# Optimization experiments

Hardware: AMD Instinct MI355X
Metric: run time of the kernel (lower is better)

Reference implementation:

```python
import jax, jax.numpy as jnp
import numpy as np

NEG_SLOPE = 0.01  # torch leaky_relu default

def _lrelu(x):
    return jax.nn.leaky_relu(x, NEG_SLOPE)

def _l2norm(x, axis):
    # torch F.normalize(p=2, eps=1e-12)
    n = jnp.linalg.norm(x, axis=axis, keepdims=True)
    return x / jnp.maximum(n, 1e-12)

def setup_inputs() -> dict:
    key = jax.random.key(0)
    ks = jax.random.split(key, 12)
    Nda, Nq, C, Din, Dout = 10000, 64, 1024, 128, 256
    target_adj = (jax.random.uniform(ks[0], (Nda, Nda)) < 0.002).astype(jnp.float32)
    query_adj = (jax.random.uniform(ks[1], (Nq, Nq)) < 0.2).astype(jnp.float32)
    node_features_da = jax.random.normal(ks[2], (Nda, Din), dtype=jnp.float32)
    node_features_q = jax.random.normal(ks[3], (Nq, Din), dtype=jnp.float32)
    candidate_set = jax.random.randint(ks[4], (C,), 0, Nda)
    candidate_adj = (jax.random.uniform(ks[5], (C, C)) < 0.01).astype(jnp.float32)
    s_in = 1.0 / np.sqrt(Din).astype(np.float32)
    s_out = 1.0 / np.sqrt(Dout).astype(np.float32)
    W1_da = jax.random.normal(ks[6], (Din, Dout), dtype=jnp.float32) * s_in
    W1_q = jax.random.normal(ks[7], (Din, Dout), dtype=jnp.float32) * s_in
    W2_da = jax.random.normal(ks[8], (Dout, Dout), dtype=jnp.float32) * s_out
    W2_q = jax.random.normal(ks[9], (Dout, Dout), dtype=jnp.float32) * s_out
    threshold = jnp.float32(0.2)
    return {"target_adj": target_adj, "node_features_da": node_features_da,
            "query_adj": query_adj, "node_features_q": node_features_q,
            "candidate_set": candidate_set, "candidate_adj": candidate_adj,
            "threshold": threshold, "W1_da": W1_da, "W1_q": W1_q,
            "W2_da": W2_da, "W2_q": W2_q}

def _cross_cosine(q, da, candidate_set):
    # cosine similarity between each query node and each candidate target node: [Nq, C]
    return _l2norm(q, 1) @ _l2norm(da[candidate_set], 1).T

def reference(target_adj, node_features_da, query_adj, node_features_q,
              candidate_set, candidate_adj, threshold, W1_da, W1_q, W2_da, W2_q):
    # layer 1: GCN propagation on both graphs (gcn(adj,x) = adj @ x @ W)
    da1 = _lrelu(target_adj @ (node_features_da @ W1_da))   # [Nda, D]
    q1 = _lrelu(query_adj @ (node_features_q @ W1_q))       # [Nq, D]
    c1 = _cross_cosine(q1, da1, candidate_set)               # [Nq, C]
    pre_da1 = da1[candidate_set]                             # [C, D]
    # NOTE: da1[candidate_set].data = ... mutates a temporary in torch -> no-op on da1
    att_da1 = _lrelu(da1)                                    # dropout in eval = identity
    h1_q = c1 @ pre_da1                                      # [Nq, D]
    att_q1 = _lrelu(q1 + _l2norm(h1_q, 0))
    # layer 2
    da2 = _lrelu(target_adj @ (att_da1 @ W2_da))
    q2 = _lrelu(query_adj @ (att_q1 @ W2_q))
    c2 = _cross_cosine(q2, da2, candidate_set)
    pre_da2 = da2[candidate_set]
    att_da2 = _lrelu(da2)                                    # in-place update is again a no-op
    h2_q = c2 @ pre_da2
    att_q2 = _lrelu(q2 + _l2norm(h2_q, 0))
    # graph-level matching score per target node
    emb = jnp.mean(att_q2, axis=0, keepdims=True)            # [1, D]
    num = att_da2 @ emb[0]                                   # [Nda]
    den = jnp.maximum(jnp.linalg.norm(att_da2, axis=1) * jnp.linalg.norm(emb), 1e-8)
    end = (num / den)[None, :]                               # [1, Nda]
    # threshold selection expressed with a mask (jit-safe, same math: excluded
    # rows/cols are zero and do not affect L2 norms, sums, or the trace)
    m = (end[0] > threshold).astype(att_da2.dtype)           # [Nda]
    F_ = att_da2 * m[:, None]
    re_adj = F_ @ F_.T                                       # [Nda, Nda]
    nor_re = _l2norm(re_adj, 1) * target_adj                 # elementwise with original adj
    cnt = jnp.sum(m)
    total = jnp.sum(nor_re)
    tr = jnp.trace(nor_re)
    has = cnt > 0
    pre_avg_degree = jnp.where(has, total / jnp.maximum(cnt, 1.0), 0.0)
    pre_avg_nodes = jnp.where(has, tr, 0.0)
    pre_density = jnp.where(has, 2.0 * total / (tr * (tr - 1.0) + 1e-4), 0.0)
    return (end, att_da2, att_q2, pre_avg_degree, pre_density, pre_avg_nodes)
```

## Files before the change

kernel.cpp:

```cpp
#include <hip/hip_runtime.h>

constexpr int NDA = 10000;
constexpr int NQ  = 64;
constexpr int CND = 1024;
constexpr int DIN = 128;
constexpr int D   = 256;
constexpr int CAP = 96;
constexpr int NB_BIG = ((NDA + 63) / 64) * (D / 64);

#define LRELU(x) ((x) >= 0.f ? (x) : 0.01f * (x))

__device__ __forceinline__ float wave_red64(float v) {
#pragma unroll
    for (int o = 32; o; o >>= 1) v += __shfl_down(v, o);
    return v;
}

struct GemmSmem { float As[32][68]; float Bs[32][68]; };

template <bool RELU_A, bool RELU_C>
__device__ __forceinline__ void gemm_body(GemmSmem& sm, int bx, int by,
                                          const float* __restrict__ A,
                                          const float* __restrict__ B,
                                          float* __restrict__ C,
                                          int M, int N, int K) {
    const int bm = bx * 64, bn = by * 64;
    const int tid = threadIdx.x;
    const int tx = tid & 15, ty = tid >> 4;
    const int lm = tid >> 2, lk = (tid & 3) * 8;
    const int kb = tid >> 3, nb = (tid & 7) * 8;
    const bool aValid = (bm + lm) < M;
    const float* aPtr = A + (size_t)(bm + lm) * K + lk;
    const float* bPtr = B + (size_t)kb * N + bn + nb;
    float4 ra0 = make_float4(0.f, 0.f, 0.f, 0.f), ra1 = ra0, rb0, rb1;
    if (aValid) { ra0 = *(const float4*)aPtr; ra1 = *(const float4*)(aPtr + 4); }
    rb0 = *(const float4*)bPtr;
    rb1 = *(const float4*)(bPtr + 4);
    float acc[4][4] = {};
    for (int k0 = 0; k0 < K; k0 += 32) {
        float4 wa0 = ra0, wa1 = ra1, wb0 = rb0, wb1 = rb1;
        if (RELU_A) {
            wa0.x = LRELU(wa0.x); wa0.y = LRELU(wa0.y); wa0.z = LRELU(wa0.z); wa0.w = LRELU(wa0.w);
            wa1.x = LRELU(wa1.x); wa1.y = LRELU(wa1.y); wa1.z = LRELU(wa1.z); wa1.w = LRELU(wa1.w);
        }
        sm.As[lk + 0][lm] = wa0.x; sm.As[lk + 1][lm] = wa0.y;
        sm.As[lk + 2][lm] = wa0.z; sm.As[lk + 3][lm] = wa0.w;
        sm.As[lk + 4][lm] = wa1.x; sm.As[lk + 5][lm] = wa1.y;
        sm.As[lk + 6][lm] = wa1.z; sm.As[lk + 7][lm] = wa1.w;
        *(float4*)&sm.Bs[kb][nb]     = wb0;
        *(float4*)&sm.Bs[kb][nb + 4] = wb1;
        __syncthreads();
        if (k0 + 32 < K) {
            if (aValid) {
                ra0 = *(const float4*)(aPtr + k0 + 32);
                ra1 = *(const float4*)(aPtr + k0 + 36);
            }
            rb0 = *(const float4*)(bPtr + (size_t)(k0 + 32) * N);
            rb1 = *(const float4*)(bPtr + (size_t)(k0 + 32) * N + 4);
        }
#pragma unroll
        for (int kk = 0; kk < 32; kk++) {
            float av[4], bv[4];
#pragma unroll
            for (int i = 0; i < 4; i++) av[i] = sm.As[kk][ty * 4 + i];
#pragma unroll
            for (int j = 0; j < 4; j++) bv[j] = sm.Bs[kk][tx * 4 + j];
#pragma unroll
            for (int i = 0; i < 4; i++)
#pragma unroll
                for (int j = 0; j < 4; j++) acc[i][j] += av[i] * bv[j];
        }
        __syncthreads();
    }
#pragma unroll
    for (int i = 0; i < 4; i++) {
        int r = bm + ty * 4 + i;
        if (r < M) {
            float4 v = make_float4(acc[i][0], acc[i][1], acc[i][2], acc[i][3]);
            if (RELU_C) { v.x = LRELU(v.x); v.y = LRELU(v.y); v.z = LRELU(v.z); v.w = LRELU(v.w); }
            *(float4*)(C + (size_t)r * N + bn + tx * 4) = v;
        }
    }
}

__device__ __forceinline__ void csr_body(const float* __restrict__ adj,
                                         int* __restrict__ cols,
                                         int* __restrict__ rowcnt, int row) {
    __shared__ int scnt;
    if (threadIdx.x == 0) scnt = 0;
    __syncthreads();
    const float4* rp = (const float4*)(adj + (size_t)row * NDA);
    for (int i = threadIdx.x; i < NDA / 4; i += 256) {
        float4 v = rp[i];
        if (v.x != 0.f) { int s = atomicAdd(&scnt, 1); if (s < CAP) cols[row * CAP + s] = 4 * i; }
        if (v.y != 0.f) { int s = atomicAdd(&scnt, 1); if (s < CAP) cols[row * CAP + s] = 4 * i + 1; }
        if (v.z != 0.f) { int s = atomicAdd(&scnt, 1); if (s < CAP) cols[row * CAP + s] = 4 * i + 2; }
        if (v.w != 0.f) { int s = atomicAdd(&scnt, 1); if (s < CAP) cols[row * CAP + s] = 4 * i + 3; }
    }
    __syncthreads();
    if (threadIdx.x == 0) rowcnt[row] = min(scnt, CAP);
}

__device__ __forceinline__ void spmm_body(const int* __restrict__ cols,
                                          const int* __restrict__ rowcnt,
                                          const float* __restrict__ X,
                                          float* __restrict__ out1,
                                          float* __restrict__ out2, int row) {
    int d = threadIdx.x;
    int cnt = rowcnt[row];
    __shared__ int sc[CAP];
    if (d < cnt) sc[d] = cols[row * CAP + d];
    __syncthreads();
    float a0 = 0.f, a1 = 0.f, a2 = 0.f, a3 = 0.f;
    int k = 0;
    for (; k + 4 <= cnt; k += 4) {
        a0 += X[(size_t)sc[k + 0] * D + d];
        a1 += X[(size_t)sc[k + 1] * D + d];
        a2 += X[(size_t)sc[k + 2] * D + d];
        a3 += X[(size_t)sc[k + 3] * D + d];
    }
    for (; k < cnt; k++) a0 += X[(size_t)sc[k] * D + d];
    float v = LRELU(a0 + a1 + a2 + a3);
    out1[(size_t)row * D + d] = v;
    if (out2) out2[(size_t)row * D + d] = LRELU(v);
}

__global__ __launch_bounds__(256) void stage0_kernel(const float* __restrict__ adj,
                                                     int* __restrict__ cols,
                                                     int* __restrict__ rowcnt,
                                                     const float* __restrict__ Fda,
                                                     const float* __restrict__ W1da,
                                                     float* __restrict__ X1,
                                                     const float* __restrict__ Fq,
                                                     const float* __restrict__ W1q,
                                                     float* __restrict__ Xq) {
    __shared__ GemmSmem gs;
    int bid = blockIdx.x;
    if (bid < NB_BIG) {
        gemm_body<false, false>(gs, bid >> 2, bid & 3, Fda, W1da, X1, NDA, D, DIN);
    } else if (bid < NB_BIG + 4) {
        gemm_body<false, false>(gs, 0, bid - NB_BIG, Fq, W1q, Xq, NQ, D, DIN);
    } else {
        csr_body(adj, cols, rowcnt, bid - (NB_BIG + 4));
    }
}

__global__ __launch_bounds__(256) void stage_sg_kernel(const int* __restrict__ cols,
                                                       const int* __restrict__ rowcnt,
                                                       const float* __restrict__ X,
                                                       float* __restrict__ out1,
                                                       float* __restrict__ out2,
                                                       const float* __restrict__ Aq,
                                                       const float* __restrict__ Bq,
                                                       float* __restrict__ Cq) {
    __shared__ GemmSmem gs;
    int bid = blockIdx.x;
    if (bid < 4) {
        gemm_body<false, true>(gs, 0, bid, Aq, Bq, Cq, NQ, D, NQ);
    } else {
        spmm_body(cols, rowcnt, X, out1, out2, bid - 4);
    }
}

__global__ __launch_bounds__(256) void stage4_kernel(const float* __restrict__ da1,
                                                     const float* __restrict__ W2da,
                                                     float* __restrict__ Y2,
                                                     const float* __restrict__ aq1,
                                                     const float* __restrict__ W2q,
                                                     float* __restrict__ Zq) {
    __shared__ GemmSmem gs;
    int bid = blockIdx.x;
    if (bid < NB_BIG) {
        gemm_body<true, false>(gs, bid >> 2, bid & 3, da1, W2da, Y2, NDA, D, D);
    } else {
        gemm_body<false, false>(gs, 0, bid - NB_BIG, aq1, W2q, Zq, NQ, D, D);
    }
}

__global__ __launch_bounds__(256) void gemmH_kernel(const float* __restrict__ A,
                                                    const float* __restrict__ B,
                                                    float* __restrict__ C) {
    __shared__ GemmSmem gs;
    gemm_body<false, false>(gs, blockIdx.x, blockIdx.y, A, B, C, NDA, D, D);
}

__global__ __launch_bounds__(256) void cross_kernel(const float* __restrict__ q,
                                                    const float* __restrict__ da,
                                                    const int* __restrict__ cand,
                                                    float* __restrict__ hpart) {
    __shared__ float qs[D];
    __shared__ float cmw[256];
    __shared__ int sci[256];
    __shared__ float red[4];
    __shared__ float sqn;
    int r = blockIdx.x, qr = blockIdx.y;
    int d = threadIdx.x;
    float qv = q[r * D + d];
    qs[d] = qv;
    sci[d] = cand[qr * 256 + d];
    float p = wave_red64(qv * qv);
    int w = d >> 6, lane = d & 63;
    if (lane == 0) red[w] = p;
    __syncthreads();
    if (d == 0) sqn = fmaxf(sqrtf(red[0] + red[1] + red[2] + red[3]), 1e-12f);
    __syncthreads();
    float qn = sqn;
    {
        const float4* ap = (const float4*)(da + (size_t)sci[d] * D);
        float dot = 0.f, sq = 0.f;
#pragma unroll 8
        for (int k = 0; k < D / 4; k++) {
            float4 v = ap[k];
            dot += qs[4 * k] * v.x + qs[4 * k + 1] * v.y + qs[4 * k + 2] * v.z + qs[4 * k + 3] * v.w;
            sq  += v.x * v.x + v.y * v.y + v.z * v.z + v.w * v.w;
        }
        cmw[d] = dot / (qn * fmaxf(sqrtf(sq), 1e-12f));
    }
    __syncthreads();
    float a0 = 0.f, a1 = 0.f, a2 = 0.f, a3 = 0.f, a4 = 0.f, a5 = 0.f, a6 = 0.f, a7 = 0.f;
    for (int c = 0; c < 256; c += 8) {
        a0 += cmw[c + 0] * da[(size_t)sci[c + 0] * D + d];
        a1 += cmw[c + 1] * da[(size_t)sci[c + 1] * D + d];
        a2 += cmw[c + 2] * da[(size_t)sci[c + 2] * D + d];
        a3 += cmw[c + 3] * da[(size_t)sci[c + 3] * D + d];
        a4 += cmw[c + 4] * da[(size_t)sci[c + 4] * D + d];
        a5 += cmw[c + 5] * da[(size_t)sci[c + 5] * D + d];
        a6 += cmw[c + 6] * da[(size_t)sci[c + 6] * D + d];
        a7 += cmw[c + 7] * da[(size_t)sci[c + 7] * D + d];
    }
    hpart[((size_t)qr * NQ + r) * D + d] = ((a0 + a1) + (a2 + a3)) + ((a4 + a5) + (a6 + a7));
}

__global__ __launch_bounds__(256) void attq_kernel(const float* __restrict__ q,
                                                   const float* __restrict__ hpart,
                                                   float* __restrict__ attq,
                                                   float* __restrict__ emb) {
    int d = threadIdx.x;
    float hv[NQ];
    float ss = 0.f;
#pragma unroll
    for (int r = 0; r < NQ; r++) {
        float h = hpart[(size_t)r * D + d]
                + hpart[(size_t)(NQ + r) * D + d]
                + hpart[(size_t)(2 * NQ + r) * D + d]
                + hpart[(size_t)(3 * NQ + r) * D + d];
        hv[r] = h;
        ss += h * h;
    }
    float inv = 1.f / fmaxf(sqrtf(ss), 1e-12f);
    float es = 0.f;
#pragma unroll
    for (int r = 0; r < NQ; r++) {
        float v = q[r * D + d] + hv[r] * inv;
        v = LRELU(v);
        attq[r * D + d] = v;
        es += v;
    }
    if (emb) {
        float e = es * (1.f / (float)NQ);
        emb[d] = e;
        float p = wave_red64(e * e);
        __shared__ float red[4];
        int w = d >> 6, lane = d & 63;
        if (lane == 0) red[w] = p;
        __syncthreads();
        if (d == 0) emb[D] = sqrtf(red[0] + red[1] + red[2] + red[3]);
    }
}

__global__ __launch_bounds__(256) void end_kernel(const float* __restrict__ A,
                                                  const float* __restrict__ emb,
                                                  const float* __restrict__ thr_p,
                                                  float* __restrict__ endv,
                                                  float* __restrict__ m,
                                                  float* __restrict__ cnt) {
    __shared__ float se[D];
    __shared__ float scnt;
    int d = threadIdx.x;
    se[d] = emb[d];
    if (d == 0) scnt = 0.f;
    __syncthreads();
    float embn = emb[D];
    float thr = *thr_p;
    int w = d >> 6, lane = d & 63;
    int row = blockIdx.x * 4 + w;
    const float* ar = A + (size_t)row * D;
    float num = 0.f, sq = 0.f;
#pragma unroll
    for (int s = 0; s < 4; s++) {
        float v = ar[lane + 64 * s];
        num += v * se[lane + 64 * s];
        sq += v * v;
    }
#pragma unroll
    for (int o = 32; o; o >>= 1) { num += __shfl_down(num, o); sq += __shfl_down(sq, o); }
    if (lane == 0) {
        float den = fmaxf(sqrtf(sq) * embn, 1e-8f);
        float e = num / den;
        endv[row] = e;
        float mv = e > thr ? 1.f : 0.f;
        m[row] = mv;
        if (mv != 0.f) atomicAdd(&scnt, 1.f);
    }
    __syncthreads();
    if (d == 0 && scnt != 0.f) atomicAdd(cnt, scnt);
}

constexpr int GCHUNK = 400;
__global__ __launch_bounds__(256) void G_kernel(const float* __restrict__ A,
                                                const float* __restrict__ m,
                                                float* __restrict__ G) {
    __shared__ float SA[8][64], SB[8][64];
    int ti = blockIdx.x >> 2, tj = blockIdx.x & 3;
    int base = blockIdx.y * GCHUNK;
    int tid = threadIdx.x;
    int tx = tid & 15, ty = tid >> 4;
    float acc[4][4] = {};
    for (int g0 = 0; g0 < GCHUNK; g0 += 8) {
        for (int l = tid; l < 512; l += 256) {
            int rr = l >> 6, c = l & 63;
            int r = base + g0 + rr;
            float mv = m[r];
            SA[rr][c] = A[(size_t)r * D + ti * 64 + c] * mv;
            SB[rr][c] = A[(size_t)r * D + tj * 64 + c];
        }
        __syncthreads();
#pragma unroll
        for (int rr = 0; rr < 8; rr++) {
            float av[4], bv[4];
#pragma unroll
            for (int i = 0; i < 4; i++) av[i] = SA[rr][ty * 4 + i];
#pragma unroll
            for (int j = 0; j < 4; j++) bv[j] = SB[rr][tx * 4 + j];
#pragma unroll
            for (int i = 0; i < 4; i++)
#pragma unroll
                for (int j = 0; j < 4; j++) acc[i][j] += av[i] * bv[j];
        }
        __syncthreads();
    }
#pragma unroll
    for (int i = 0; i < 4; i++)
#pragma unroll
        for (int j = 0; j < 4; j++)
            atomicAdd(&G[(ti * 64 + ty * 4 + i) * D + tj * 64 + tx * 4 + j], acc[i][j]);
}

__global__ __launch_bounds__(256) void final_kernel(const int* __restrict__ cols,
                                                    const int* __restrict__ rowcnt,
                                                    const float* __restrict__ m,
                                                    const float* __restrict__ A,
                                                    const float* __restrict__ H,
                                                    double* __restrict__ total,
                                                    double* __restrict__ tr) {
    int i = blockIdx.x;
    if (m[i] == 0.f) return;
    int d = threadIdx.x;
    int cnt = rowcnt[i];
    __shared__ int sc[CAP];
    __shared__ float smask[CAP];
    __shared__ int sdiag;
    __shared__ float r1[4], r2[4], r3[4];
    if (d == 0) sdiag = 0;
    if (d < cnt) {
        int j = cols[i * CAP + d];
        sc[d] = j;
        smask[d] = m[j];
        if (j == i) sdiag = 1;
    }
    __syncthreads();
    float av = A[(size_t)i * D + d];
    float hv = H[(size_t)i * D + d];
    float sd = 0.f;
    for (int k = 0; k < cnt; k++)
        if (smask[k] != 0.f) sd += A[(size_t)sc[k] * D + d];
    float p1 = av * sd, p2 = av * hv, p3 = av * av;
#pragma unroll
    for (int o = 32; o; o >>= 1) {
        p1 += __shfl_down(p1, o);
        p2 += __shfl_down(p2, o);
        p3 += __shfl_down(p3, o);
    }
    int w = d >> 6, lane = d & 63;
    if (lane == 0) { r1[w] = p1; r2[w] = p2; r3[w] = p3; }
    __syncthreads();
    if (d == 0) {
        float num  = r1[0] + r1[1] + r1[2] + r1[3];
        float den2 = r2[0] + r2[1] + r2[2] + r2[3];
        float self = r3[0] + r3[1] + r3[2] + r3[3];
        float denom = fmaxf(sqrtf(den2), 1e-12f);
        double inv = 1.0 / (double)denom;
        if (num != 0.f) atomicAdd(total, (double)num * inv);
        if (sdiag) atomicAdd(tr, (double)self * inv);
    }
}

__global__ void scalars_kernel(const float* __restrict__ cnt,
                               const double* __restrict__ total,
                               const double* __restrict__ tr,
                               float* __restrict__ out) {
    float c = *cnt;
    float T = (float)*total;
    float R = (float)*tr;
    bool has = c > 0.f;
    out[0] = has ? (T / fmaxf(c, 1.f)) : 0.f;
    out[1] = has ? (2.f * T / (R * (R - 1.f) + 1e-4f)) : 0.f;
    out[2] = has ? R : 0.f;
}

extern "C" void kernel_launch(void* const* d_in, const int* in_sizes, int n_in,
                              void* d_out, int out_size, void* d_ws, size_t ws_size,
                              hipStream_t stream) {
    (void)in_sizes; (void)n_in; (void)out_size; (void)ws_size;
    const float* adj  = (const float*)d_in[0];
    const float* Fda  = (const float*)d_in[1];
    const float* Qadj = (const float*)d_in[2];
    const float* Fq   = (const float*)d_in[3];
    const int*   cand = (const int*)d_in[4];
    const float* thr  = (const float*)d_in[6];
    const float* W1da = (const float*)d_in[7];
    const float* W1q  = (const float*)d_in[8];
    const float* W2da = (const float*)d_in[9];
    const float* W2q  = (const float*)d_in[10];

    float* out = (float*)d_out;
    float* o_end    = out;
    float* o_attda2 = out + NDA;
    float* o_attq2  = out + NDA + (size_t)NDA * D;
    float* o_sc     = o_attq2 + NQ * D;

    char* w = (char*)d_ws;
    size_t off = 0;
    auto alloc = [&](size_t b) { size_t r = off; off += (b + 255) & ~(size_t)255; return r; };
    float* bufA = (float*)(w + alloc((size_t)NDA * D * 4));
    float* bufB = (float*)(w + alloc((size_t)NDA * D * 4));
    float* bufC = (float*)(w + alloc((size_t)NDA * D * 4));
    int* colsb   = (int*)(w + alloc((size_t)NDA * CAP * 4));
    int* rowcntb = (int*)(w + alloc((size_t)NDA * 4));
    float* mbuf  = (float*)(w + alloc((size_t)NDA * 4));
    char* zbase = w + alloc(262144 + 256);
    float* Gb    = (float*)zbase;
    float* cntb  = (float*)(zbase + 262144);
    double* totb = (double*)(zbase + 262144 + 8);
    double* trb  = (double*)(zbase + 262144 + 16);
    float* xq   = (float*)(w + alloc((size_t)NQ * D * 4));
    float* q1b  = (float*)(w + alloc((size_t)NQ * D * 4));
    float* aq1  = (float*)(w + alloc((size_t)NQ * D * 4));
    float* q2b  = (float*)(w + alloc((size_t)NQ * D * 4));
    float* hpart = (float*)(w + alloc((size_t)4 * NQ * D * 4));
    float* embb = (float*)(w + alloc((size_t)(D + 1) * 4));

    hipMemsetAsync(zbase, 0, 262144 + 256, stream);

    stage0_kernel<<<NB_BIG + 4 + NDA, 256, 0, stream>>>(adj, colsb, rowcntb,
                                                        Fda, W1da, bufA,
                                                        Fq, W1q, xq);
    stage_sg_kernel<<<NDA + 4, 256, 0, stream>>>(colsb, rowcntb, bufA, bufB, (float*)nullptr,
                                                 Qadj, xq, q1b);
    cross_kernel<<<dim3(NQ, 4), 256, 0, stream>>>(q1b, bufB, cand, hpart);
    attq_kernel<<<1, 256, 0, stream>>>(q1b, hpart, aq1, (float*)nullptr);
    stage4_kernel<<<NB_BIG + 4, 256, 0, stream>>>(bufB, W2da, bufA, aq1, W2q, xq);
    stage_sg_kernel<<<NDA + 4, 256, 0, stream>>>(colsb, rowcntb, bufA, bufC, o_attda2,
                                                 Qadj, xq, q2b);
    cross_kernel<<<dim3(NQ, 4), 256, 0, stream>>>(q2b, bufC, cand, hpart);
    attq_kernel<<<1, 256, 0, stream>>>(q2b, hpart, o_attq2, embb);
    end_kernel<<<NDA / 4, 256, 0, stream>>>(o_attda2, embb, thr, o_end, mbuf, cntb);
    G_kernel<<<dim3(16, NDA / GCHUNK), 256, 0, stream>>>(o_attda2, mbuf, Gb);
    gemmH_kernel<<<dim3((NDA + 63) / 64, D / 64), 256, 0, stream>>>(o_attda2, Gb, bufB);
    final_kernel<<<NDA, 256, 0, stream>>>(colsb, rowcntb, mbuf, o_attda2, bufB, totb, trb);
    scalars_kernel<<<1, 1, 0, stream>>>(cntb, totb, trb, o_sc);
}
```

Before: 1.050 ms.

## Fuse pipeline into one cooperative persistent kernel with grid syncs

Replaces the chain of separate kernel launches with a single cooperative persistent megakernel that walks through the stages with grid-wide syncs, sharing one shared-memory union. Multi-launch code is kept as a fallback. It also splits the G accumulation into per-chunk partials plus a reduction instead of global atomics, and merges the first cross-similarity with the second-layer GEMM. The aim is to cut launch gaps and atomic contention, at the cost of grid sync overhead and lower occupancy for the large stages.

```diff
diff --git a/kernel.cpp b/kernel.cpp
--- a/kernel.cpp
+++ b/kernel.cpp
@@ -1,4 +1,7 @@
 #include <hip/hip_runtime.h>
+#include <hip/hip_cooperative_groups.h>
+
+namespace cg = cooperative_groups;
 
 constexpr int NDA = 10000;
 constexpr int NQ  = 64;
@@ -7,6 +10,8 @@
 constexpr int D   = 256;
 constexpr int CAP = 96;
 constexpr int NB_BIG = ((NDA + 63) / 64) * (D / 64);
+constexpr int NCHUNK = 16;
+constexpr int GCHUNK = 640;
 
 #define LRELU(x) ((x) >= 0.f ? (x) : 0.01f * (x))
 
@@ -16,7 +21,18 @@
     return v;
 }
 
-struct GemmSmem { float As[32][68]; float Bs[32][68]; };
+struct GemmSmem  { float As[32][68]; float Bs[32][68]; };
+struct CrossSmem { float qs[D]; float cmw[256]; int sci[256]; float red[4]; float sqn; };
+struct SpmmSmem  { int sc[CAP]; };
+struct CsrSmem   { int scnt; };
+struct EndSmem   { float se[D]; float scnt; };
+struct FinalSmem { int sc[CAP]; float smask[CAP]; int sdiag; float r1[4], r2[4], r3[4]; };
+struct GpSmem    { float SA[8][64]; float SB[8][64]; };
+struct AttqSmem  { float red[4]; };
+union SMem {
+    GemmSmem g; CrossSmem c; SpmmSmem s; CsrSmem z;
+    EndSmem e; FinalSmem f; GpSmem gp; AttqSmem a;
+};
 
 template <bool RELU_A, bool RELU_C>
 __device__ __forceinline__ void gemm_body(GemmSmem& sm, int bx, int by,
@@ -83,175 +99,111 @@
     }
 }
 
-__device__ __forceinline__ void csr_body(const float* __restrict__ adj,
+__device__ __forceinline__ void csr_body(CsrSmem& sm, const float* __restrict__ adj,
                                          int* __restrict__ cols,
                                          int* __restrict__ rowcnt, int row) {
-    __shared__ int scnt;
-    if (threadIdx.x == 0) scnt = 0;
+    if (threadIdx.x == 0) sm.scnt = 0;
     __syncthreads();
     const float4* rp = (const float4*)(adj + (size_t)row * NDA);
     for (int i = threadIdx.x; i < NDA / 4; i += 256) {
         float4 v = rp[i];
-        if (v.x != 0.f) { int s = atomicAdd(&scnt, 1); if (s < CAP) cols[row * CAP + s] = 4 * i; }
-        if (v.y != 0.f) { int s = atomicAdd(&scnt, 1); if (s < CAP) cols[row * CAP + s] = 4 * i + 1; }
-        if (v.z != 0.f) { int s = atomicAdd(&scnt, 1); if (s < CAP) cols[row * CAP + s] = 4 * i + 2; }
-        if (v.w != 0.f) { int s = atomicAdd(&scnt, 1); if (s < CAP) cols[row * CAP + s] = 4 * i + 3; }
-    }
-    __syncthreads();
-    if (threadIdx.x == 0) rowcnt[row] = min(scnt, CAP);
-}
-
-__device__ __forceinline__ void spmm_body(const int* __restrict__ cols,
+        if (v.x != 0.f) { int s = atomicAdd(&sm.scnt, 1); if (s < CAP) cols[row * CAP + s] = 4 * i; }
+        if (v.y != 0.f) { int s = atomicAdd(&sm.scnt, 1); if (s < CAP) cols[row * CAP + s] = 4 * i + 1; }
+        if (v.z != 0.f) { int s = atomicAdd(&sm.scnt, 1); if (s < CAP) cols[row * CAP + s] = 4 * i + 2; }
+        if (v.w != 0.f) { int s = atomicAdd(&sm.scnt, 1); if (s < CAP) cols[row * CAP + s] = 4 * i + 3; }
+    }
+    __syncthreads();
+    if (threadIdx.x == 0) rowcnt[row] = min(sm.scnt, CAP);
+}
+
+__device__ __forceinline__ void spmm_body(SpmmSmem& sm, const int* __restrict__ cols,
                                           const int* __restrict__ rowcnt,
                                           const float* __restrict__ X,
                                           float* __restrict__ out1,
                                           float* __restrict__ out2, int row) {
     int d = threadIdx.x;
     int cnt = rowcnt[row];
-    __shared__ int sc[CAP];
-    if (d < cnt) sc[d] = cols[row * CAP + d];
+    if (d < cnt) sm.sc[d] = cols[row * CAP + d];
     __syncthreads();
     float a0 = 0.f, a1 = 0.f, a2 = 0.f, a3 = 0.f;
     int k = 0;
     for (; k + 4 <= cnt; k += 4) {
-        a0 += X[(size_t)sc[k + 0] * D + d];
-        a1 += X[(size_t)sc[k + 1] * D + d];
-        a2 += X[(size_t)sc[k + 2] * D + d];
-        a3 += X[(size_t)sc[k + 3] * D + d];
-    }
-    for (; k < cnt; k++) a0 += X[(size_t)sc[k] * D + d];
+        a0 += X[(size_t)sm.sc[k + 0] * D + d];
+        a1 += X[(size_t)sm.sc[k + 1] * D + d];
+        a2 += X[(size_t)sm.sc[k + 2] * D + d];
+        a3 += X[(size_t)sm.sc[k + 3] * D + d];
+    }
+    for (; k < cnt; k++) a0 += X[(size_t)sm.sc[k] * D + d];
     float v = LRELU(a0 + a1 + a2 + a3);
     out1[(size_t)row * D + d] = v;
     if (out2) out2[(size_t)row * D + d] = LRELU(v);
 }
 
-__global__ __launch_bounds__(256) void stage0_kernel(const float* __restrict__ adj,
-                                                     int* __restrict__ cols,
-                                                     int* __restrict__ rowcnt,
-                                                     const float* __restrict__ Fda,
-                                                     const float* __restrict__ W1da,
-                                                     float* __restrict__ X1,
-                                                     const float* __restrict__ Fq,
-                                                     const float* __restrict__ W1q,
-                                                     float* __restrict__ Xq) {
-    __shared__ GemmSmem gs;
-    int bid = blockIdx.x;
-    if (bid < NB_BIG) {
-        gemm_body<false, false>(gs, bid >> 2, bid & 3, Fda, W1da, X1, NDA, D, DIN);
-    } else if (bid < NB_BIG + 4) {
-        gemm_body<false, false>(gs, 0, bid - NB_BIG, Fq, W1q, Xq, NQ, D, DIN);
-    } else {
-        csr_body(adj, cols, rowcnt, bid - (NB_BIG + 4));
-    }
-}
-
-__global__ __launch_bounds__(256) void stage_sg_kernel(const int* __restrict__ cols,
-                                                       const int* __restrict__ rowcnt,
-                                                       const float* __restrict__ X,
-                                                       float* __restrict__ out1,
-                                                       float* __restrict__ out2,
-                                                       const float* __restrict__ Aq,
-                                                       const float* __restrict__ Bq,
-                                                       float* __restrict__ Cq) {
-    __shared__ GemmSmem gs;
-    int bid = blockIdx.x;
-    if (bid < 4) {
-        gemm_body<false, true>(gs, 0, bid, Aq, Bq, Cq, NQ, D, NQ);
-    } else {
-        spmm_body(cols, rowcnt, X, out1, out2, bid - 4);
-    }
-}
-
-__global__ __launch_bounds__(256) void stage4_kernel(const float* __restrict__ da1,
-                                                     const float* __restrict__ W2da,
-                                                     float* __restrict__ Y2,
-                                                     const float* __restrict__ aq1,
-                                                     const float* __restrict__ W2q,
-                                                     float* __restrict__ Zq) {
-    __shared__ GemmSmem gs;
-    int bid = blockIdx.x;
-    if (bid < NB_BIG) {
-        gemm_body<true, false>(gs, bid >> 2, bid & 3, da1, W2da, Y2, NDA, D, D);
-    } else {
-        gemm_body<false, false>(gs, 0, bid - NB_BIG, aq1, W2q, Zq, NQ, D, D);
-    }
-}
-
-__global__ __launch_bounds__(256) void gemmH_kernel(const float* __restrict__ A,
-                                                    const float* __restrict__ B,
-                                                    float* __restrict__ C) {
-    __shared__ GemmSmem gs;
-    gemm_body<false, false>(gs, blockIdx.x, blockIdx.y, A, B, C, NDA, D, D);
-}
-
-__global__ __launch_bounds__(256) void cross_kernel(const float* __restrict__ q,
-                                                    const float* __restrict__ da,
-                                                    const int* __restrict__ cand,
-                                                    float* __restrict__ hpart) {
-    __shared__ float qs[D];
-    __shared__ float cmw[256];
-    __shared__ int sci[256];
-    __shared__ float red[4];
-    __shared__ float sqn;
-    int r = blockIdx.x, qr = blockIdx.y;
+__device__ __forceinline__ void cross_body(CrossSmem& sm, const float* __restrict__ q,
+                                           const float* __restrict__ da,
+                                           const int* __restrict__ cand,
+                                           float* __restrict__ hpart,
+                                           int r, int qr) {
     int d = threadIdx.x;
     float qv = q[r * D + d];
-    qs[d] = qv;
-    sci[d] = cand[qr * 256 + d];
+    sm.qs[d] = qv;
+    sm.sci[d] = cand[qr * 256 + d];
     float p = wave_red64(qv * qv);
     int w = d >> 6, lane = d & 63;
-    if (lane == 0) red[w] = p;
-    __syncthreads();
-    if (d == 0) sqn = fmaxf(sqrtf(red[0] + red[1] + red[2] + red[3]), 1e-12f);
-    __syncthreads();
-    float qn = sqn;
+    if (lane == 0) sm.red[w] = p;
+    __syncthreads();
+    if (d == 0) sm.sqn = fmaxf(sqrtf(sm.red[0] + sm.red[1] + sm.red[2] + sm.red[3]), 1e-12f);
+    __syncthreads();
+    float qn = sm.sqn;
     {
-        const float4* ap = (const float4*)(da + (size_t)sci[d] * D);
+        const float4* ap = (const float4*)(da + (size_t)sm.sci[d] * D);
         float dot = 0.f, sq = 0.f;
 #pragma unroll 8
         for (int k = 0; k < D / 4; k++) {
             float4 v = ap[k];
-            dot += qs[4 * k] * v.x + qs[4 * k + 1] * v.y + qs[4 * k + 2] * v.z + qs[4 * k + 3] * v.w;
+            dot += sm.qs[4 * k] * v.x + sm.qs[4 * k + 1] * v.y + sm.qs[4 * k + 2] * v.z + sm.qs[4 * k + 3] * v.w;
             sq  += v.x * v.x + v.y * v.y + v.z * v.z + v.w * v.w;
         }
-        cmw[d] = dot / (qn * fmaxf(sqrtf(sq), 1e-12f));
+        sm.cmw[d] = dot / (qn * fmaxf(sqrtf(sq), 1e-12f));
     }
     __syncthreads();
     float a0 = 0.f, a1 = 0.f, a2 = 0.f, a3 = 0.f, a4 = 0.f, a5 = 0.f, a6 = 0.f, a7 = 0.f;
     for (int c = 0; c < 256; c += 8) {
-        a0 += cmw[c + 0] * da[(size_t)sci[c + 0] * D + d];
-        a1 += cmw[c + 1] * da[(size_t)sci[c + 1] * D + d];
-        a2 += cmw[c + 2] * da[(size_t)sci[c + 2] * D + d];
-        a3 += cmw[c + 3] * da[(size_t)sci[c + 3] * D + d];
-        a4 += cmw[c + 4] * da[(size_t)sci[c + 4] * D + d];
-        a5 += cmw[c + 5] * da[(size_t)sci[c + 5] * D + d];
-        a6 += cmw[c + 6] * da[(size_t)sci[c + 6] * D + d];
-        a7 += cmw[c + 7] * da[(size_t)sci[c + 7] * D + d];
+        a0 += sm.cmw[c + 0] * da[(size_t)sm.sci[c + 0] * D + d];
+        a1 += sm.cmw[c + 1] * da[(size_t)sm.sci[c + 1] * D + d];
+        a2 += sm.cmw[c + 2] * da[(size_t)sm.sci[c + 2] * D + d];
+        a3 += sm.cmw[c + 3] * da[(size_t)sm.sci[c + 3] * D + d];
+        a4 += sm.cmw[c + 4] * da[(size_t)sm.sci[c + 4] * D + d];
+        a5 += sm.cmw[c + 5] * da[(size_t)sm.sci[c + 5] * D + d];
+        a6 += sm.cmw[c + 6] * da[(size_t)sm.sci[c + 6] * D + d];
+        a7 += sm.cmw[c + 7] * da[(size_t)sm.sci[c + 7] * D + d];
     }
     hpart[((size_t)qr * NQ + r) * D + d] = ((a0 + a1) + (a2 + a3)) + ((a4 + a5) + (a6 + a7));
 }
 
-__global__ __launch_bounds__(256) void attq_kernel(const float* __restrict__ q,
-                                                   const float* __restrict__ hpart,
-                                                   float* __restrict__ attq,
-                                                   float* __restrict__ emb) {
+__device__ __forceinline__ void attq_body(AttqSmem& sm, const float* __restrict__ q,
+                                          const float* __restrict__ hpart,
+                                          float* __restrict__ attq,
+                                          float* __restrict__ emb) {
     int d = threadIdx.x;
-    float hv[NQ];
     float ss = 0.f;
-#pragma unroll
+#pragma unroll 4
     for (int r = 0; r < NQ; r++) {
         float h = hpart[(size_t)r * D + d]
                 + hpart[(size_t)(NQ + r) * D + d]
                 + hpart[(size_t)(2 * NQ + r) * D + d]
                 + hpart[(size_t)(3 * NQ + r) * D + d];
-        hv[r] = h;
         ss += h * h;
     }
     float inv = 1.f / fmaxf(sqrtf(ss), 1e-12f);
     float es = 0.f;
-#pragma unroll
+#pragma unroll 4
     for (int r = 0; r < NQ; r++) {
-        float v = q[r * D + d] + hv[r] * inv;
+        float h = hpart[(size_t)r * D + d]
+                + hpart[(size_t)(NQ + r) * D + d]
+                + hpart[(size_t)(2 * NQ + r) * D + d]
+                + hpart[(size_t)(3 * NQ + r) * D + d];
+        float v = q[r * D + d] + h * inv;
         v = LRELU(v);
         attq[r * D + d] = v;
         es += v;
@@ -260,36 +212,33 @@
         float e = es * (1.f / (float)NQ);
         emb[d] = e;
         float p = wave_red64(e * e);
-        __shared__ float red[4];
         int w = d >> 6, lane = d & 63;
-        if (lane == 0) red[w] = p;
-        __syncthreads();
-        if (d == 0) emb[D] = sqrtf(red[0] + red[1] + red[2] + red[3]);
-    }
-}
-
-__global__ __launch_bounds__(256) void end_kernel(const float* __restrict__ A,
-                                                  const float* __restrict__ emb,
-                                                  const float* __restrict__ thr_p,
-                                                  float* __restrict__ endv,
-                                                  float* __restrict__ m,
-                                                  float* __restrict__ cnt) {
-    __shared__ float se[D];
-    __shared__ float scnt;
+        if (lane == 0) sm.red[w] = p;
+        __syncthreads();
+        if (d == 0) emb[D] = sqrtf(sm.red[0] + sm.red[1] + sm.red[2] + sm.red[3]);
+    }
+}
+
+__device__ __forceinline__ void end_body(EndSmem& sm, const float* __restrict__ A,
+                                         const float* __restrict__ emb,
+                                         const float* __restrict__ thr_p,
+                                         float* __restrict__ endv,
+                                         float* __restrict__ m,
+                                         float* __restrict__ cnt, int quad) {
     int d = threadIdx.x;
-    se[d] = emb[d];
-    if (d == 0) scnt = 0.f;
+    sm.se[d] = emb[d];
+    if (d == 0) sm.scnt = 0.f;
     __syncthreads();
     float embn = emb[D];
     float thr = *thr_p;
     int w = d >> 6, lane = d & 63;
-    int row = blockIdx.x * 4 + w;
+    int row = quad * 4 + w;
     const float* ar = A + (size_t)row * D;
     float num = 0.f, sq = 0.f;
 #pragma unroll
     for (int s = 0; s < 4; s++) {
         float v = ar[lane + 64 * s];
-        num += v * se[lane + 64 * s];
+        num += v * sm.se[lane + 64 * s];
         sq += v * v;
     }
 #pragma unroll
@@ -300,19 +249,17 @@
         endv[row] = e;
         float mv = e > thr ? 1.f : 0.f;
         m[row] = mv;
-        if (mv != 0.f) atomicAdd(&scnt, 1.f);
-    }
-    __syncthreads();
-    if (d == 0 && scnt != 0.f) atomicAdd(cnt, scnt);
-}
-
-constexpr int GCHUNK = 400;
-__global__ __launch_bounds__(256) void G_kernel(const float* __restrict__ A,
-                                                const float* __restrict__ m,
-                                                float* __restrict__ G) {
-    __shared__ float SA[8][64], SB[8][64];
-    int ti = blockIdx.x >> 2, tj = blockIdx.x & 3;
-    int base = blockIdx.y * GCHUNK;
+        if (mv != 0.f) atomicAdd(&sm.scnt, 1.f);
+    }
+    __syncthreads();
+    if (d == 0 && sm.scnt != 0.f) atomicAdd(cnt, sm.scnt);
+}
+
+__device__ __forceinline__ void gpart_body(GpSmem& sm, const float* __restrict__ A,
+                                           const float* __restrict__ m,
+                                           float* __restrict__ Gp, int tile, int chunk) {
+    int ti = tile >> 2, tj = tile & 3;
+    int base = chunk * GCHUNK;
     int tid = threadIdx.x;
     int tx = tid & 15, ty = tid >> 4;
     float acc[4][4] = {};
@@ -320,18 +267,23 @@
         for (int l = tid; l < 512; l += 256) {
             int rr = l >> 6, c = l & 63;
             int r = base + g0 + rr;
-            float mv = m[r];
-            SA[rr][c] = A[(size_t)r * D + ti * 64 + c] * mv;
-            SB[rr][c] = A[(size_t)r * D + tj * 64 + c];
+            float av = 0.f, bv = 0.f, mv = 0.f;
+            if (r < NDA) {
+                mv = m[r];
+                av = A[(size_t)r * D + ti * 64 + c];
+                bv = A[(size_t)r * D + tj * 64 + c];
+            }
+            sm.SA[rr][c] = av * mv;
+            sm.SB[rr][c] = bv;
         }
         __syncthreads();
 #pragma unroll
         for (int rr = 0; rr < 8; rr++) {
             float av[4], bv[4];
 #pragma unroll
-            for (int i = 0; i < 4; i++) av[i] = SA[rr][ty * 4 + i];
-#pragma unroll
-            for (int j = 0; j < 4; j++) bv[j] = SB[rr][tx * 4 + j];
+            for (int i = 0; i < 4; i++) av[i] = sm.SA[rr][ty * 4 + i];
+#pragma unroll
+            for (int j = 0; j < 4; j++) bv[j] = sm.SB[rr][tx * 4 + j];
 #pragma unroll
             for (int i = 0; i < 4; i++)
 #pragma unroll
@@ -339,41 +291,37 @@
         }
         __syncthreads();
     }
+    float* gp = Gp + (size_t)chunk * D * D;
 #pragma unroll
     for (int i = 0; i < 4; i++)
 #pragma unroll
         for (int j = 0; j < 4; j++)
-            atomicAdd(&G[(ti * 64 + ty * 4 + i) * D + tj * 64 + tx * 4 + j], acc[i][j]);
-}
-
-__global__ __launch_bounds__(256) void final_kernel(const int* __restrict__ cols,
-                                                    const int* __restrict__ rowcnt,
-                                                    const float* __restrict__ m,
-                                                    const float* __restrict__ A,
-                                                    const float* __restrict__ H,
-                                                    double* __restrict__ total,
-                                                    double* __restrict__ tr) {
-    int i = blockIdx.x;
+            gp[(ti * 64 + ty * 4 + i) * D + tj * 64 + tx * 4 + j] = acc[i][j];
+}
+
+__device__ __forceinline__ void final_body(FinalSmem& sm, const int* __restrict__ cols,
+                                           const int* __restrict__ rowcnt,
+                                           const float* __restrict__ m,
+                                           const float* __restrict__ A,
+                                           const float* __restrict__ H,
+                                           double* __restrict__ total,
+                                           double* __restrict__ tr, int i) {
     if (m[i] == 0.f) return;
     int d = threadIdx.x;
     int cnt = rowcnt[i];
-    __shared__ int sc[CAP];
-    __shared__ float smask[CAP];
-    __shared__ int sdiag;
-    __shared__ float r1[4], r2[4], r3[4];
-    if (d == 0) sdiag = 0;
+    if (d == 0) sm.sdiag = 0;
     if (d < cnt) {
         int j = cols[i * CAP + d];
-        sc[d] = j;
-        smask[d] = m[j];
-        if (j == i) sdiag = 1;
+        sm.sc[d] = j;
+        sm.smask[d] = m[j];
+        if (j == i) sm.sdiag = 1;
     }
     __syncthreads();
     float av = A[(size_t)i * D + d];
     float hv = H[(size_t)i * D + d];
     float sd = 0.f;
     for (int k = 0; k < cnt; k++)
-        if (smask[k] != 0.f) sd += A[(size_t)sc[k] * D + d];
+        if (sm.smask[k] != 0.f) sd += A[(size_t)sm.sc[k] * D + d];
     float p1 = av * sd, p2 = av * hv, p3 = av * av;
 #pragma unroll
     for (int o = 32; o; o >>= 1) {
@@ -382,23 +330,188 @@
         p3 += __shfl_down(p3, o);
     }
     int w = d >> 6, lane = d & 63;
-    if (lane == 0) { r1[w] = p1; r2[w] = p2; r3[w] = p3; }
+    if (lane == 0) { sm.r1[w] = p1; sm.r2[w] = p2; sm.r3[w] = p3; }
     __syncthreads();
     if (d == 0) {
-        float num  = r1[0] + r1[1] + r1[2] + r1[3];
-        float den2 = r2[0] + r2[1] + r2[2] + r2[3];
-        float self = r3[0] + r3[1] + r3[2] + r3[3];
+        float num  = sm.r1[0] + sm.r1[1] + sm.r1[2] + sm.r1[3];
+        float den2 = sm.r2[0] + sm.r2[1] + sm.r2[2] + sm.r2[3];
+        float self = sm.r3[0] + sm.r3[1] + sm.r3[2] + sm.r3[3];
         float denom = fmaxf(sqrtf(den2), 1e-12f);
         double inv = 1.0 / (double)denom;
         if (num != 0.f) atomicAdd(total, (double)num * inv);
-        if (sdiag) atomicAdd(tr, (double)self * inv);
-    }
-}
-
-__global__ void scalars_kernel(const float* __restrict__ cnt,
-                               const double* __restrict__ total,
-                               const double* __restrict__ tr,
-                               float* __restrict__ out) {
+        if (sm.sdiag) atomicAdd(tr, (double)self * inv);
+    }
+}
+
+struct P {
+    const float *adj, *Fda, *Qadj, *Fq;
+    const int* cand;
+    const float* thr;
+    const float *W1da, *W1q, *W2da, *W2q;
+    float *o_end, *o_attda2, *o_attq2, *o_sc;
+    float *bufA, *bufB, *bufC;
+    int *cols, *rowcnt;
+    float *m, *Gb, *Gp;
+    float* cnt; double *tot, *tr;
+    float *xq, *q1, *aq1, *q2, *hpart, *emb;
+};
+
+__global__ __launch_bounds__(256) void mega(P p) {
+    cg::grid_group grid = cg::this_grid();
+    __shared__ SMem sm;
+    const int nb = gridDim.x;
+    const int b0 = blockIdx.x;
+    if (b0 == 0 && threadIdx.x == 0) { *p.cnt = 0.f; *p.tot = 0.0; *p.tr = 0.0; }
+    for (int it = b0; it < NB_BIG + 4 + NDA; it += nb) {
+        if (it < NB_BIG) gemm_body<false, false>(sm.g, it >> 2, it & 3, p.Fda, p.W1da, p.bufA, NDA, D, DIN);
+        else if (it < NB_BIG + 4) gemm_body<false, false>(sm.g, 0, it - NB_BIG, p.Fq, p.W1q, p.xq, NQ, D, DIN);
+        else csr_body(sm.z, p.adj, p.cols, p.rowcnt, it - (NB_BIG + 4));
+        __syncthreads();
+    }
+    grid.sync();
+    for (int it = b0; it < 4 + NDA; it += nb) {
+        if (it < 4) gemm_body<false, true>(sm.g, 0, it, p.Qadj, p.xq, p.q1, NQ, D, NQ);
+        else spmm_body(sm.s, p.cols, p.rowcnt, p.bufA, p.bufB, nullptr, it - 4);
+        __syncthreads();
+    }
+    grid.sync();
+    for (int it = b0; it < 256 + NB_BIG; it += nb) {
+        if (it < 256) cross_body(sm.c, p.q1, p.bufB, p.cand, p.hpart, it >> 2, it & 3);
+        else { int t = it - 256; gemm_body<true, false>(sm.g, t >> 2, t & 3, p.bufB, p.W2da, p.bufA, NDA, D, D); }
+        __syncthreads();
+    }
+    grid.sync();
+    for (int it = b0; it < 1 + 5000; it += nb) {
+        if (it == 0) attq_body(sm.a, p.q1, p.hpart, p.aq1, nullptr);
+        else spmm_body(sm.s, p.cols, p.rowcnt, p.bufA, p.bufC, p.o_attda2, it - 1);
+        __syncthreads();
+    }
+    grid.sync();
+    for (int it = b0; it < 4 + 5000; it += nb) {
+        if (it < 4) gemm_body<false, false>(sm.g, 0, it, p.aq1, p.W2q, p.xq, NQ, D, D);
+        else spmm_body(sm.s, p.cols, p.rowcnt, p.bufA, p.bufC, p.o_attda2, 5000 + (it - 4));
+        __syncthreads();
+    }
+    grid.sync();
+    for (int it = b0; it < 4; it += nb) {
+        gemm_body<false, true>(sm.g, 0, it, p.Qadj, p.xq, p.q2, NQ, D, NQ);
+        __syncthreads();
+    }
+    grid.sync();
+    for (int it = b0; it < 256; it += nb) {
+        cross_body(sm.c, p.q2, p.bufC, p.cand, p.hpart, it >> 2, it & 3);
+        __syncthreads();
+    }
+    grid.sync();
+    for (int it = b0; it < 1; it += nb) {
+        attq_body(sm.a, p.q2, p.hpart, p.o_attq2, p.emb);
+        __syncthreads();
+    }
+    grid.sync();
+    for (int it = b0; it < NDA / 4; it += nb) {
+        end_body(sm.e, p.o_attda2, p.emb, p.thr, p.o_end, p.m, p.cnt, it);
+        __syncthreads();
+    }
+    grid.sync();
+    for (int it = b0; it < 16 * NCHUNK; it += nb) {
+        gpart_body(sm.gp, p.o_attda2, p.m, p.Gp, it & 15, it >> 4);
+        __syncthreads();
+    }
+    grid.sync();
+    for (int it = b0; it < (D * D) / 256; it += nb) {
+        int idx = it * 256 + (int)threadIdx.x;
+        float s = 0.f;
+#pragma unroll
+        for (int c2 = 0; c2 < NCHUNK; c2++) s += p.Gp[(size_t)c2 * D * D + idx];
+        p.Gb[idx] = s;
+    }
+    grid.sync();
+    for (int it = b0; it < NB_BIG; it += nb) {
+        gemm_body<false, false>(sm.g, it >> 2, it & 3, p.o_attda2, p.Gb, p.bufB, NDA, D, D);
+        __syncthreads();
+    }
+    grid.sync();
+    for (int it = b0; it < NDA; it += nb) {
+        final_body(sm.f, p.cols, p.rowcnt, p.m, p.o_attda2, p.bufB, p.tot, p.tr, it);
+        __syncthreads();
+    }
+    grid.sync();
+    if (b0 == 0 && threadIdx.x == 0) {
+        float c = *p.cnt;
+        float T = (float)*p.tot;
+        float R = (float)*p.tr;
+        bool has = c > 0.f;
+        p.o_sc[0] = has ? (T / fmaxf(c, 1.f)) : 0.f;
+        p.o_sc[1] = has ? (2.f * T / (R * (R - 1.f) + 1e-4f)) : 0.f;
+        p.o_sc[2] = has ? R : 0.f;
+    }
+}
+
+__global__ __launch_bounds__(256) void k_stage0(const float* adj, int* cols, int* rowcnt,
+                                                const float* Fda, const float* W1da, float* X1,
+                                                const float* Fq, const float* W1q, float* Xq) {
+    __shared__ SMem sm;
+    int bid = blockIdx.x;
+    if (bid < NB_BIG) gemm_body<false, false>(sm.g, bid >> 2, bid & 3, Fda, W1da, X1, NDA, D, DIN);
+    else if (bid < NB_BIG + 4) gemm_body<false, false>(sm.g, 0, bid - NB_BIG, Fq, W1q, Xq, NQ, D, DIN);
+    else csr_body(sm.z, adj, cols, rowcnt, bid - (NB_BIG + 4));
+}
+__global__ __launch_bounds__(256) void k_sg(const int* cols, const int* rowcnt, const float* X,
+                                            float* out1, float* out2,
+                                            const float* Aq, const float* Bq, float* Cq) {
+    __shared__ SMem sm;
+    int bid = blockIdx.x;
+    if (bid < 4) gemm_body<false, true>(sm.g, 0, bid, Aq, Bq, Cq, NQ, D, NQ);
+    else spmm_body(sm.s, cols, rowcnt, X, out1, out2, bid - 4);
+}
+__global__ __launch_bounds__(256) void k_mergeA(const float* q1, const float* da1, const int* cand,
+                                                float* hpart, const float* W2da, float* Y2) {
+    __shared__ SMem sm;
+    int bid = blockIdx.x;
+    if (bid < 256) cross_body(sm.c, q1, da1, cand, hpart, bid >> 2, bid & 3);
+    else { int t = bid - 256; gemm_body<true, false>(sm.g, t >> 2, t & 3, da1, W2da, Y2, NDA, D, D); }
+}
+__global__ __launch_bounds__(256) void k_cross(const float* q, const float* da, const int* cand,
+                                               float* hpart) {
+    __shared__ SMem sm;
+    cross_body(sm.c, q, da, cand, hpart, blockIdx.x, blockIdx.y);
+}
+__global__ __launch_bounds__(256) void k_attq(const float* q, const float* hpart, float* attq,
+                                              float* emb) {
+    __shared__ SMem sm;
+    attq_body(sm.a, q, hpart, attq, emb);
+}
+__global__ __launch_bounds__(256) void k_gemmZ(const float* A, const float* B, float* C) {
+    __shared__ SMem sm;
+    gemm_body<false, false>(sm.g, 0, blockIdx.x, A, B, C, NQ, D, D);
+}
+__global__ __launch_bounds__(256) void k_end(const float* A, const float* emb, const float* thr,
+                                             float* endv, float* m, float* cnt) {
+    __shared__ SMem sm;
+    end_body(sm.e, A, emb, thr, endv, m, cnt, blockIdx.x);
+}
+__global__ __launch_bounds__(256) void k_gpart(const float* A, const float* m, float* Gp) {
+    __shared__ SMem sm;
+    gpart_body(sm.gp, A, m, Gp, blockIdx.x, blockIdx.y);
+}
+__global__ __launch_bounds__(256) void k_gred(const float* Gp, float* G) {
+    int idx = blockIdx.x * 256 + threadIdx.x;
+    float s = 0.f;
+#pragma unroll
+    for (int c = 0; c < NCHUNK; c++) s += Gp[(size_t)c * D * D + idx];
+    G[idx] = s;
+}
+__global__ __launch_bounds__(256) void k_gemmH(const float* A, const float* B, float* C) {
+    __shared__ SMem sm;
+    gemm_body<false, false>(sm.g, blockIdx.x, blockIdx.y, A, B, C, NDA, D, D);
+}
+__global__ __launch_bounds__(256) void k_final(const int* cols, const int* rowcnt, const float* m,
+                                               const float* A, const float* H,
+                                               double* total, double* tr) {
+    __shared__ SMem sm;
+    final_body(sm.f, cols, rowcnt, m, A, H, total, tr, blockIdx.x);
+}
+__global__ void k_scalars(const float* cnt, const double* total, const double* tr, float* out) {
     float c = *cnt;
     float T = (float)*total;
     float R = (float)*tr;
@@ -438,11 +551,12 @@
     int* colsb   = (int*)(w + alloc((size_t)NDA * CAP * 4));
     int* rowcntb = (int*)(w + alloc((size_t)NDA * 4));
     float* mbuf  = (float*)(w + alloc((size_t)NDA * 4));
-    char* zbase = w + alloc(262144 + 256);
-    float* Gb    = (float*)zbase;
-    float* cntb  = (float*)(zbase + 262144);
-    double* totb = (double*)(zbase + 262144 + 8);
-    double* trb  = (double*)(zbase + 262144 + 16);
+    float* Gb    = (float*)(w + alloc((size_t)D * D * 4));
+    float* Gp    = (float*)(w + alloc((size_t)NCHUNK * D * D * 4));
+    char* zbase = w + alloc(256);
+    float* cntb  = (float*)zbase;
+    double* totb = (double*)(zbase + 8);
+    double* trb  = (double*)(zbase + 16);
     float* xq   = (float*)(w + alloc((size_t)NQ * D * 4));
     float* q1b  = (float*)(w + alloc((size_t)NQ * D * 4));
     float* aq1  = (float*)(w + alloc((size_t)NQ * D * 4));
@@ -450,23 +564,44 @@
     float* hpart = (float*)(w + alloc((size_t)4 * NQ * D * 4));
     float* embb = (float*)(w + alloc((size_t)(D + 1) * 4));
 
-    hipMemsetAsync(zbase, 0, 262144 + 256, stream);
-
-    stage0_kernel<<<NB_BIG + 4 + NDA, 256, 0, stream>>>(adj, colsb, rowcntb,
-                                                        Fda, W1da, bufA,
-                                                        Fq, W1q, xq);
-    stage_sg_kernel<<<NDA + 4, 256, 0, stream>>>(colsb, rowcntb, bufA, bufB, (float*)nullptr,
-                                                 Qadj, xq, q1b);
-    cross_kernel<<<dim3(NQ, 4), 256, 0, stream>>>(q1b, bufB, cand, hpart);
-    attq_kernel<<<1, 256, 0, stream>>>(q1b, hpart, aq1, (float*)nullptr);
-    stage4_kernel<<<NB_BIG + 4, 256, 0, stream>>>(bufB, W2da, bufA, aq1, W2q, xq);
-    stage_sg_kernel<<<NDA + 4, 256, 0, stream>>>(colsb, rowcntb, bufA, bufC, o_attda2,
-                                                 Qadj, xq, q2b);
-    cross_kernel<<<dim3(NQ, 4), 256, 0, stream>>>(q2b, bufC, cand, hpart);
-    attq_kernel<<<1, 256, 0, stream>>>(q2b, hpart, o_attq2, embb);
-    end_kernel<<<NDA / 4, 256, 0, stream>>>(o_attda2, embb, thr, o_end, mbuf, cntb);
-    G_kernel<<<dim3(16, NDA / GCHUNK), 256, 0, stream>>>(o_attda2, mbuf, Gb);
-    gemmH_kernel<<<dim3((NDA + 63) / 64, D / 64), 256, 0, stream>>>(o_attda2, Gb, bufB);
-    final_kernel<<<NDA, 256, 0, stream>>>(colsb, rowcntb, mbuf, o_attda2, bufB, totb, trb);
-    scalars_kernel<<<1, 1, 0, stream>>>(cntb, totb, trb, o_sc);
-}
+    static int grid_blocks = 0;
+    if (grid_blocks == 0) {
+        int bpc = 0;
+        if (hipOccupancyMaxActiveBlocksPerMultiprocessor(&bpc, mega, 256, 0) != hipSuccess || bpc <= 0)
+            bpc = 2;
+        hipDeviceProp_t prop;
+        int ncu = 256;
+        if (hipGetDeviceProperties(&prop, 0) == hipSuccess && prop.multiProcessorCount > 0)
+            ncu = prop.multiProcessorCount;
+        grid_blocks = bpc * ncu;
+        if (grid_blocks > 4096) grid_blocks = 4096;
+        if (grid_blocks < 64) grid_blocks = 64;
+    }
+
+    P p = { adj, Fda, Qadj, Fq, cand, thr, W1da, W1q, W2da, W2q,
+            o_end, o_attda2, o_attq2, o_sc,
+            bufA, bufB, bufC, colsb, rowcntb,
+            mbuf, Gb, Gp, cntb, totb, trb,
+            xq, q1b, aq1, q2b, hpart, embb };
+    void* args[] = { &p };
+    hipError_t ce = hipLaunchCooperativeKernel((const void*)mega, dim3(grid_blocks), dim3(256),
+                                               args, 0u, stream);
+    if (ce == hipSuccess) return;
+    (void)hipGetLastError();
+
+    hipMemsetAsync(zbase, 0, 256, stream);
+    k_stage0<<<NB_BIG + 4 + NDA, 256, 0, stream>>>(adj, colsb, rowcntb, Fda, W1da, bufA, Fq, W1q, xq);
+    k_sg<<<NDA + 4, 256, 0, stream>>>(colsb, rowcntb, bufA, bufB, (float*)nullptr, Qadj, xq, q1b);
+    k_mergeA<<<256 + NB_BIG, 256, 0, stream>>>(q1b, bufB, cand, hpart, W2da, bufA);
+    k_attq<<<1, 256, 0, stream>>>(q1b, hpart, aq1, (float*)nullptr);
+    k_gemmZ<<<4, 256, 0, stream>>>(aq1, W2q, xq);
+    k_sg<<<NDA + 4, 256, 0, stream>>>(colsb, rowcntb, bufA, bufC, o_attda2, Qadj, xq, q2b);
+    k_cross<<<dim3(NQ, 4), 256, 0, stream>>>(q2b, bufC, cand, hpart);
+    k_attq<<<1, 256, 0, stream>>>(q2b, hpart, o_attq2, embb);
+    k_end<<<NDA / 4, 256, 0, stream>>>(o_attda2, embb, thr, o_end, mbuf, cntb);
+    k_gpart<<<dim3(16, NCHUNK), 256, 0, stream>>>(o_attda2, mbuf, Gp);
+    k_gred<<<D * D / 256, 256, 0, stream>>>(Gp, Gb);
+    k_gemmH<<<dim3((NDA + 63) / 64, D / 64), 256, 0, stream>>>(o_attda2, Gb, bufB);
+    k_final<<<NDA, 256, 0, stream>>>(colsb, rowcntb, mbuf, o_attda2, bufB, totb, trb);
+    k_scalars<<<1, 1, 0, stream>>>(cntb, totb, trb, o_sc);
+}
```

After: 1.790 ms. 70.5% more time.
